# Optimization experiments

Hardware: AMD Instinct MI355X
Metric: run time of the kernel (lower is better)

## Reference

```python
import jax, jax.numpy as jnp
import numpy as np

# dims
T, B, N, H = 16, 8, 8, 128            # time, batch, num_schemas, schema_dim
C, IH, IW = 32, 16, 16                # conv_dims
TASK, ACT, REW = 128, 16, 1
HEADS = 7
TAR = TASK + ACT + REW                # 145
CTX = H + TAR                         # 273 context_dim
CONV_FLAT = C * IH * IW               # 8192
MEM_IN = CONV_FLAT + H + CTX          # 8593


def setup_inputs() -> dict:
    key = jax.random.key(0)
    ks = jax.random.split(key, 20)
    def n(k, shape, s=0.02):
        return jax.random.normal(k, shape, dtype=jnp.float32) * s
    D = HEADS * H
    return {
        "image": jax.random.normal(ks[0], (T, B, C, IH, IW), dtype=jnp.float32),
        "task_action_reward": jax.random.normal(ks[1], (T, B, TAR), dtype=jnp.float32),
        # MultiHeadedAttention params
        "Wq_w": n(ks[2], (D, CTX)), "Wq_b": jnp.zeros((D,), jnp.float32),
        "Wk_w": n(ks[3], (D, H)),   "Wk_b": jnp.zeros((D,), jnp.float32),
        "Wv_w": n(ks[4], (D, H)),   "Wv_b": jnp.zeros((D,), jnp.float32),
        "Wo_w": n(ks[5], (H, D)),   "Wo_b": jnp.zeros((H,), jnp.float32),
        # TopdownFeatureAttention: N per-query linears (stacked) + 1x1 conv
        "td_w": n(ks[6], (N, C, CTX)), "td_b": jnp.zeros((N, C), jnp.float32),
        "conv_w": n(ks[7], (C, C)), "conv_b": jnp.zeros((C,), jnp.float32),
        # ListStructuredRnn: N per-schema LSTM cells (PyTorch gate order i,f,g,o)
        "Wih": n(ks[8], (N, 4 * H, MEM_IN)), "Whh": n(ks[9], (N, 4 * H, H)),
        "bih": jnp.zeros((N, 4 * H), jnp.float32), "bhh": jnp.zeros((N, 4 * H), jnp.float32),
    }


def reference(image, task_action_reward, Wq_w, Wq_b, Wk_w, Wk_b, Wv_w, Wv_b,
              Wo_w, Wo_b, td_w, td_b, conv_w, conv_b, Wih, Whh, bih, bhh):
    f32 = image.dtype
    # prev_state=None path: prev_h is zeros for all timesteps
    prev_h = jnp.zeros((T, B, N, H), f32)
    # schema_context = duplicate task_action_reward over schemas, cat prev_h -> (T,B,N,CTX)
    ctx = jnp.concatenate(
        [jnp.broadcast_to(task_action_reward[:, :, None, :], (T, B, N, TAR)), prev_h], axis=-1)
    # keys = cat(prev_h, zeros) along schema axis -> (T,B,N+1,H)
    keys = jnp.concatenate([prev_h, jnp.zeros((T, B, 1, H), f32)], axis=2)

    # --- MultiHeadedAttention (no mask; dropout unused in forward) ---
    q = (ctx @ Wq_w.T + Wq_b).reshape(T, B, N, HEADS, H)
    k = (keys @ Wk_w.T + Wk_b).reshape(T, B, N + 1, HEADS, H)
    v = (keys @ Wv_w.T + Wv_b).reshape(T, B, N + 1, HEADS, H)
    scores = jnp.einsum('tbqhd,tbkhd->tbhqk', q, k) / jnp.sqrt(jnp.asarray(H, f32))
    attn = jax.nn.softmax(scores, axis=-1)
    xatt = jnp.einsum('tbhqk,tbkhd->tbqhd', attn, v).reshape(T, B, N, HEADS * H)
    shared = xatt @ Wo_w.T + Wo_b                      # (T,B,N,H)

    # --- TopdownFeatureAttention: per-query linear -> sigmoid channel gate -> 1x1 conv ---
    gate = jax.nn.sigmoid(jnp.einsum('tbnx,ncx->tbnc', ctx, td_w) + td_b)   # (T,B,N,C)
    modulated = image[:, :, None] * gate[..., None, None]                    # (T,B,N,C,IH,IW)
    conv = jnp.einsum('tbnchw,dc->tbndhw', modulated, conv_w) + conv_b[:, None, None]
    schema_updates = conv.reshape(T, B, N, CONV_FLAT)

    # --- per-schema LSTMs over time (zero initial state) ---
    mem = jnp.concatenate([schema_updates, shared, ctx], axis=-1)            # (T,B,N,MEM_IN)
    xg = jnp.einsum('tbni,ngi->tbng', mem, Wih) + bih + bhh                  # (T,B,N,4H)

    def step(carry, g_t):
        h, c = carry
        g = g_t + jnp.einsum('bnh,ngh->bng', h, Whh)
        i, f, gg, o = jnp.split(g, 4, axis=-1)
        c = jax.nn.sigmoid(f) * c + jax.nn.sigmoid(i) * jnp.tanh(gg)
        h = jax.nn.sigmoid(o) * jnp.tanh(c)
        return (h, c), h

    z = jnp.zeros((B, N, H), f32)
    (hT, cT), hs = jax.lax.scan(step, (z, z), xg)
    outs = hs.reshape(T, B, N * H)
    return outs, hT, cT
```

## Files before the change

kernel.cpp:

```cpp
#include <hip/hip_runtime.h>

#define T_   16
#define B_   8
#define N_   8
#define H_   128
#define C_   32
#define HW_  256
#define TAR_ 145
#define G4H  512
#define MEMIN 8593
#define AK   8512
#define XGN  524288
#define KSTEP 64

typedef __attribute__((ext_vector_type(8))) short short8v;
typedef __attribute__((ext_vector_type(4))) float f32x4;
typedef __attribute__((ext_vector_type(4), aligned(4))) float f32x4u;

__device__ __forceinline__ float bf2f(unsigned short u){
  return __uint_as_float(((unsigned int)u) << 16);
}
__device__ __forceinline__ unsigned short f2bf(float x){
  unsigned int b = __float_as_uint(x);
  return (unsigned short)((b + 0x7fffu + ((b >> 16) & 1u)) >> 16);
}
__device__ __forceinline__ unsigned pkbf(float lo, float hi){
  return __builtin_amdgcn_perm(__float_as_uint(hi) + 0x8000u,
                               __float_as_uint(lo) + 0x8000u, 0x07060302u);
}
__device__ __forceinline__ float bflo(unsigned w){ return __uint_as_float(w << 16); }
__device__ __forceinline__ float bfhi(unsigned w){ return __uint_as_float(w & 0xffff0000u); }
__device__ __forceinline__ float sigf(float x){ return 1.f/(1.f + expf(-x)); }

__device__ __forceinline__ void gl_lds16(const void* g, void* l){
  __builtin_amdgcn_global_load_lds(
      (const __attribute__((address_space(1))) unsigned int*)g,
      (__attribute__((address_space(3))) unsigned int*)l, 16, 0, 0);
}
__device__ __forceinline__ void gl_lds4(const void* g, void* l){
  __builtin_amdgcn_global_load_lds(
      (const __attribute__((address_space(1))) unsigned int*)g,
      (__attribute__((address_space(3))) unsigned int*)l, 4, 0, 0);
}

__global__ void k_shared(const float* __restrict__ WvB, const float* __restrict__ WoW,
                         const float* __restrict__ WoB, float* __restrict__ sh){
  const int h = blockIdx.x, lane = threadIdx.x;
  float acc = 0.f;
  for(int d = lane; d < 896; d += 64) acc += WvB[d] * WoW[h*896 + d];
  for(int s = 32; s; s >>= 1) acc += __shfl_down(acc, s);
  if(lane == 0) sh[h] = acc + WoB[h];
}

__global__ __launch_bounds__(256) void k_gate(const float* __restrict__ tar,
                                              const float* __restrict__ tdw,
                                              const float* __restrict__ tdb,
                                              float* __restrict__ gate){
  __shared__ float twS[32*145];
  __shared__ float taS[16*145];
  const int tb0 = blockIdx.x * 16, n = blockIdx.y, tid = threadIdx.x;
  for(int i = tid; i < 32*145; i += 256){
    int c = i / 145, x = i - c*145;
    twS[i] = tdw[(n*32 + c)*273 + x];
  }
  for(int i = tid; i < 16*145; i += 256)
    taS[i] = tar[tb0*145 + i];
  __syncthreads();
  for(int o = tid; o < 512; o += 256){
    int r = o >> 5, c = o & 31;
    float a = tdb[n*32 + c];
    const float* tr = &taS[r*145];
    const float* tw = &twS[c*145];
    for(int x = 0; x < 145; ++x) a += tr[x]*tw[x];
    gate[((tb0 + r)*N_ + n)*C_ + c] = 1.f/(1.f + expf(-a));
  }
}

__global__ __launch_bounds__(256) void k_conv2(
    const float* __restrict__ img, const float* __restrict__ gate,
    const float* __restrict__ cw, const float* __restrict__ cb,
    const float* __restrict__ sh, const float* __restrict__ tar,
    unsigned short* __restrict__ mem)
{
  __shared__ float imgS[8192];
  __shared__ float cwgT[1024];
  const int tb = blockIdx.x, n = blockIdx.y;
  const int hw = threadIdx.x;
  for(int i = hw; i < 8192; i += 256)
    imgS[i] = img[(size_t)tb*8192 + i];
  for(int i = hw; i < 1024; i += 256){
    const int c = i >> 5, d = i & 31;
    cwgT[i] = cw[d*32 + c] * gate[(tb*8 + n)*32 + c];
  }
  __syncthreads();
  f32x4 acc[8];
  #pragma unroll
  for(int dq = 0; dq < 8; ++dq){
    const f32x4u cv = *(const f32x4u*)&cb[dq*4];
    acc[dq].x = cv.x; acc[dq].y = cv.y; acc[dq].z = cv.z; acc[dq].w = cv.w;
  }
  #pragma unroll 4
  for(int c = 0; c < 32; ++c){
    const float iv = imgS[c*256 + hw];
    #pragma unroll
    for(int dq = 0; dq < 8; ++dq){
      const f32x4 w = *(const f32x4*)&cwgT[c*32 + dq*4];
      acc[dq].x += iv*w.x; acc[dq].y += iv*w.y;
      acc[dq].z += iv*w.z; acc[dq].w += iv*w.w;
    }
  }
  unsigned short* mrow = mem + (size_t)(n*128 + tb)*AK;
  #pragma unroll
  for(int dq = 0; dq < 8; ++dq){
    mrow[(dq*4 + 0)*256 + hw] = f2bf(acc[dq].x);
    mrow[(dq*4 + 1)*256 + hw] = f2bf(acc[dq].y);
    mrow[(dq*4 + 2)*256 + hw] = f2bf(acc[dq].z);
    mrow[(dq*4 + 3)*256 + hw] = f2bf(acc[dq].w);
  }
  for(int i = hw; i < 320; i += 256){
    if(i < 128)      mrow[8192 + i]       = f2bf(sh[i]);
    else if(i < 273) mrow[8320 + i - 128] = f2bf(tar[tb*TAR_ + i - 128]);
    else             mrow[8465 + i - 273] = 0;
  }
}

__global__ __launch_bounds__(256) void k_gemm7(
    const unsigned short* __restrict__ mem, const float* __restrict__ Wih,
    float* __restrict__ xg)
{
  extern __shared__ char smem7[];
  unsigned short (*Abuf)[128*64] = (unsigned short(*)[128*64])smem7;
  float (*Bbuf)[16*64] = (float(*)[16*64])(smem7 + 4*128*64*2);
  const int bid = blockIdx.x;
  const int n = bid & 7, gt = bid >> 3;
  const int tid = threadIdx.x;
  const int wv = tid >> 6, ln = tid & 63;
  const int lr = ln & 15, lg = ln >> 4;
  const int g0 = gt*16;
  const unsigned short* An = mem + (size_t)n*128*AK;
  const float* Bn = Wih + (size_t)(n*G4H + g0)*MEMIN;

#define STAGE7(sl, kk) do{                                                     \
    _Pragma("unroll")                                                          \
    for(int i_ = 0; i_ < 4; ++i_){                                             \
      const int ci_ = i_*256 + tid;                                            \
      const int row_ = ci_ >> 3;                                               \
      const unsigned short* src_ = An + (size_t)row_*AK + (kk)                 \
                                   + (((ci_ & 7) ^ (row_ & 7)) << 3);          \
      gl_lds16(src_, &Abuf[sl][(i_*256 + wv*64)*8]);                           \
    }                                                                          \
    _Pragma("unroll")                                                          \
    for(int q_ = 0; q_ < 4; ++q_){                                             \
      const int idx_ = q_*256 + tid;                                           \
      const int g_ = idx_ >> 6;                                                \
      const int kd_ = idx_ & 63;                                               \
      const float* srcB_ = Bn + (size_t)g_*MEMIN + (kk)                        \
                           + ((((kd_ >> 3) ^ (g_ & 7)) << 3) + (kd_ & 7));     \
      gl_lds4(srcB_, &Bbuf[sl][q_*256 + wv*64]);                               \
    }                                                                          \
  }while(0)

  f32x4 acc0 = {0.f,0.f,0.f,0.f};
  f32x4 acc1 = {0.f,0.f,0.f,0.f};

  STAGE7(0, 0);
  STAGE7(1, KSTEP);
  STAGE7(2, 2*KSTEP);

  for(int t = 0; t < 133; ++t){
    if(t < 131){
      asm volatile("s_waitcnt vmcnt(16)" ::: "memory");
    } else if(t == 131){
      asm volatile("s_waitcnt vmcnt(8)" ::: "memory");
    } else {
      asm volatile("s_waitcnt vmcnt(0)" ::: "memory");
    }
    __builtin_amdgcn_s_barrier();
    const int sl = t & 3;
    #pragma unroll
    for(int s = 0; s < 2; ++s){
      const int jb = (s*4 + lg) ^ (lr & 7);
      const float* bp = &Bbuf[sl][lr*64 + jb*8];
      const f32x4 blo = *(const f32x4*)bp;
      const f32x4 bhi = *(const f32x4*)(bp + 4);
      short8v bf;
      unsigned* u = (unsigned*)&bf;
      u[0] = pkbf(blo.x, blo.y); u[1] = pkbf(blo.z, blo.w);
      u[2] = pkbf(bhi.x, bhi.y); u[3] = pkbf(bhi.z, bhi.w);
      const short8v a0 = *(const short8v*)&Abuf[sl][(wv*32 + lr)*64 + jb*8];
      const short8v a1 = *(const short8v*)&Abuf[sl][(wv*32 + 16 + lr)*64 + jb*8];
      acc0 = __builtin_amdgcn_mfma_f32_16x16x32_bf16(a0, bf, acc0, 0, 0, 0);
      acc1 = __builtin_amdgcn_mfma_f32_16x16x32_bf16(a1, bf, acc1, 0, 0, 0);
    }
    if(t + 3 < 133) STAGE7((t + 3) & 3, (t + 3)*KSTEP);
  }
#undef STAGE7

  const int c0 = g0 + lr;
  const int r0 = wv*32 + lg*4, r1 = r0 + 16;
  #pragma unroll
  for(int j = 0; j < 4; ++j){
    xg[(size_t)((r0 + j)*8 + n)*G4H + c0] = acc0[j];
    xg[(size_t)((r1 + j)*8 + n)*G4H + c0] = acc1[j];
  }
}

__global__ __launch_bounds__(512) void k_lstm2(
    const float* __restrict__ xg4, int nsum, const float* __restrict__ Whh,
    const float* __restrict__ bih, const float* __restrict__ bhh,
    float* __restrict__ out)
{
  __shared__ float hS[128];
  __shared__ float preS[512];
  const int bn = blockIdx.x;
  const int n = bn & 7, b = bn >> 3;
  const int g = threadIdx.x;

  unsigned wr[64];
  const float* wrow = Whh + (size_t)(n*G4H + g)*H_;
  #pragma unroll
  for(int i = 0; i < 32; ++i){
    const f32x4 w = *(const f32x4*)(wrow + i*4);
    wr[2*i]   = pkbf(w.x, w.y);
    wr[2*i+1] = pkbf(w.z, w.w);
  }
  const float bias = bih[n*G4H + g] + bhh[n*G4H + g];
  if(g < 128) hS[g] = 0.f;
  float cc = 0.f;
  __syncthreads();

  for(int t = 0; t < 16; ++t){
    const size_t xb = (size_t)((t*8 + b)*8 + n)*G4H + g;
    float acc = bias;
    for(int u = 0; u < nsum; ++u) acc += xg4[xb + (size_t)u*XGN];
    #pragma unroll
    for(int q = 0; q < 32; ++q){
      const f32x4 hv = *(const f32x4*)&hS[q*4];
      const unsigned w0 = wr[2*q], w1 = wr[2*q+1];
      acc += hv.x*bflo(w0) + hv.y*bfhi(w0) + hv.z*bflo(w1) + hv.w*bfhi(w1);
    }
    preS[g] = acc;
    __syncthreads();
    if(g < 128){
      const float iv = sigf(preS[g]);
      const float fv = sigf(preS[128 + g]);
      const float gv = tanhf(preS[256 + g]);
      const float ov = sigf(preS[384 + g]);
      cc = fv*cc + iv*gv;
      const float hn = ov*tanhf(cc);
      hS[g] = hn;
      out[(t*8 + b)*1024 + n*128 + g] = hn;
      if(t == 15){
        out[131072 + (b*8 + n)*128 + g] = hn;
        out[139264 + (b*8 + n)*128 + g] = cc;
      }
    }
    __syncthreads();
  }
}

__global__ __launch_bounds__(256) void k_gemm5(
    const unsigned short* __restrict__ mem, const float* __restrict__ Wih,
    float* __restrict__ xg4)
{
  __shared__ unsigned short Abuf[2][128*64];
  __shared__ float          Bbuf[2][16*64];
  const int gt = blockIdx.x, n = blockIdx.y, ks = blockIdx.z;
  const int tid = threadIdx.x;
  const int wv = tid >> 6, ln = tid & 63;
  const int lr = ln & 15, lg = ln >> 4;
  const int g0 = gt*16;
  const int kbeg = (ks == 0) ? 0 : 2176 + (ks - 1)*2112;
  const int nsteps = (ks == 0) ? 34 : 33;
  const unsigned short* An = mem + (size_t)n*128*AK;
  const float* Bn = Wih + (size_t)(n*G4H + g0)*MEMIN;

#define STAGE5(bb, kk) do{                                                     \
    _Pragma("unroll")                                                          \
    for(int i_ = 0; i_ < 4; ++i_){                                             \
      const int ci_ = i_*256 + tid;                                            \
      const int row_ = ci_ >> 3;                                               \
      const unsigned short* src_ = An + (size_t)row_*AK + (kk)                 \
                                   + (((ci_ & 7) ^ (row_ & 7)) << 3);          \
      gl_lds16(src_, &Abuf[bb][(i_*256 + wv*64)*8]);                           \
    }                                                                          \
    _Pragma("unroll")                                                          \
    for(int q_ = 0; q_ < 4; ++q_){                                             \
      const int idx_ = q_*256 + tid;                                           \
      const int g_ = idx_ >> 6;                                                \
      const int kd_ = idx_ & 63;                                               \
      const float* srcB_ = Bn + (size_t)g_*MEMIN + (kk)                        \
                           + ((((kd_ >> 3) ^ (g_ & 7)) << 3) + (kd_ & 7));     \
      gl_lds4(srcB_, &Bbuf[bb][q_*256 + wv*64]);                               \
    }                                                                          \
  }while(0)

  f32x4 acc0 = {0.f,0.f,0.f,0.f};
  f32x4 acc1 = {0.f,0.f,0.f,0.f};

  STAGE5(0, kbeg);
  if(nsteps > 1) STAGE5(1, kbeg + KSTEP);

  int b = 0;
  for(int t = 0; t < nsteps; ++t){
    if(t < nsteps - 1){
      asm volatile("s_waitcnt vmcnt(8)" ::: "memory");
    } else {
      asm volatile("s_waitcnt vmcnt(0)" ::: "memory");
    }
    __builtin_amdgcn_s_barrier();
    #pragma unroll
    for(int s = 0; s < 2; ++s){
      const int jb = (s*4 + lg) ^ (lr & 7);
      const float* bp = &Bbuf[b][lr*64 + jb*8];
      const f32x4 blo = *(const f32x4*)bp;
      const f32x4 bhi = *(const f32x4*)(bp + 4);
      short8v bf;
      unsigned* u = (unsigned*)&bf;
      u[0] = pkbf(blo.x, blo.y); u[1] = pkbf(blo.z, blo.w);
      u[2] = pkbf(bhi.x, bhi.y); u[3] = pkbf(bhi.z, bhi.w);
      const short8v a0 = *(const short8v*)&Abuf[b][(wv*32 + lr)*64 + jb*8];
      const short8v a1 = *(const short8v*)&Abuf[b][(wv*32 + 16 + lr)*64 + jb*8];
      acc0 = __builtin_amdgcn_mfma_f32_16x16x32_bf16(a0, bf, acc0, 0, 0, 0);
      acc1 = __builtin_amdgcn_mfma_f32_16x16x32_bf16(a1, bf, acc1, 0, 0, 0);
    }
    __builtin_amdgcn_s_barrier();
    if(t + 2 < nsteps) STAGE5(b, kbeg + (t+2)*KSTEP);
    b ^= 1;
  }
#undef STAGE5

  float* dst = xg4 + (size_t)ks*XGN;
  const int c0 = g0 + lr;
  const int r0 = wv*32 + lg*4, r1 = r0 + 16;
  #pragma unroll
  for(int j = 0; j < 4; ++j){
    dst[(size_t)((r0 + j)*8 + n)*G4H + c0] = acc0[j];
    dst[(size_t)((r1 + j)*8 + n)*G4H + c0] = acc1[j];
  }
}

extern "C" void kernel_launch(void* const* d_in, const int* in_sizes, int n_in,
                              void* d_out, int out_size, void* d_ws, size_t ws_size,
                              hipStream_t stream)
{
  (void)in_sizes; (void)n_in; (void)out_size;
  const float* img  = (const float*)d_in[0];
  const float* tar  = (const float*)d_in[1];
  const float* WvB  = (const float*)d_in[7];
  const float* WoW  = (const float*)d_in[8];
  const float* WoB  = (const float*)d_in[9];
  const float* tdw  = (const float*)d_in[10];
  const float* tdb  = (const float*)d_in[11];
  const float* cw   = (const float*)d_in[12];
  const float* cb   = (const float*)d_in[13];
  const float* Wih  = (const float*)d_in[14];
  const float* Whh  = (const float*)d_in[15];
  const float* bih  = (const float*)d_in[16];
  const float* bhh  = (const float*)d_in[17];

  float* wsf   = (float*)d_ws;
  float* gatew = wsf;
  float* shw   = wsf + 32768;
  float* xgw   = wsf + 32896;
  unsigned short* memA = (unsigned short*)((char*)d_ws + 8520192);
  const size_t WS_7 = 8520192 + (size_t)8*128*AK*2;

  k_shared<<<128, 64, 0, stream>>>(WvB, WoW, WoB, shw);
  k_gate<<<dim3(8, 8), 256, 0, stream>>>(tar, tdw, tdb, gatew);
  k_conv2<<<dim3(128, 8), 256, 0, stream>>>(img, gatew, cw, cb, shw, tar, memA);

  if(ws_size >= WS_7){
    (void)hipFuncSetAttribute((const void*)k_gemm7,
                              hipFuncAttributeMaxDynamicSharedMemorySize, 81920);
    k_gemm7<<<256, 256, 81920, stream>>>(memA, Wih, xgw);
    k_lstm2<<<64, 512, 0, stream>>>(xgw, 1, Whh, bih, bhh, (float*)d_out);
  } else {
    k_gemm5<<<dim3(32, 8, 4), 256, 0, stream>>>(memA, Wih, xgw);
    k_lstm2<<<64, 512, 0, stream>>>(xgw, 4, Whh, bih, bhh, (float*)d_out);
  }
}
```

Measured before the change: 125.1 us.

## Widen GEMM tile to 64 gate columns with split-K over four partial outputs

Replaces the input-projection GEMM kernel with one in which each block computes 128 rows by 64 gate columns over a quarter of K, writing four partial sums that the LSTM kernel adds up (nsum=4). This lets each A tile in LDS feed eight MFMAs per wave instead of two, which cuts repeated A traffic, while split-K keeps the grid at 256 blocks. B rows are now loaded with 16-byte copies from unaligned row starts into a padded LDS layout. The cost is much more LDS per block (144KB), extra partial-sum memory traffic, and more reduction work in the LSTM kernel.

```diff
diff --git a/kernel.cpp b/kernel.cpp
--- a/kernel.cpp
+++ b/kernel.cpp
@@ -124,84 +124,94 @@
   }
 }
 
-__global__ __launch_bounds__(256) void k_gemm7(
+__global__ __launch_bounds__(256) void k_gemm8(
     const unsigned short* __restrict__ mem, const float* __restrict__ Wih,
-    float* __restrict__ xg)
-{
-  extern __shared__ char smem7[];
-  unsigned short (*Abuf)[128*64] = (unsigned short(*)[128*64])smem7;
-  float (*Bbuf)[16*64] = (float(*)[16*64])(smem7 + 4*128*64*2);
+    float* __restrict__ xg4)
+{
+  extern __shared__ char smem8[];
+  unsigned short (*Abuf)[8192] = (unsigned short(*)[8192])smem8;
+  float (*Bbuf)[5120] = (float(*)[5120])(smem8 + 4*16384);
   const int bid = blockIdx.x;
-  const int n = bid & 7, gt = bid >> 3;
+  const int n = bid & 7, r2 = bid >> 3;
+  const int gt = r2 & 7, ks = r2 >> 3;
   const int tid = threadIdx.x;
   const int wv = tid >> 6, ln = tid & 63;
   const int lr = ln & 15, lg = ln >> 4;
-  const int g0 = gt*16;
+  const int g0 = gt*64;
+  const int kbeg = (ks == 0) ? 0 : 2176 + (ks - 1)*2112;
+  const int nsteps = (ks == 0) ? 34 : 33;
   const unsigned short* An = mem + (size_t)n*128*AK;
-  const float* Bn = Wih + (size_t)(n*G4H + g0)*MEMIN;
-
-#define STAGE7(sl, kk) do{                                                     \
+  const int rbase = n*512 + g0 + wv*16;
+
+#define STAGE8(sl, kk) do{                                                     \
     _Pragma("unroll")                                                          \
     for(int i_ = 0; i_ < 4; ++i_){                                             \
       const int ci_ = i_*256 + tid;                                            \
       const int row_ = ci_ >> 3;                                               \
-      const unsigned short* src_ = An + (size_t)row_*AK + (kk)                 \
-                                   + (((ci_ & 7) ^ (row_ & 7)) << 3);          \
-      gl_lds16(src_, &Abuf[sl][(i_*256 + wv*64)*8]);                           \
+      gl_lds16(An + (size_t)row_*AK + (kk) + (((ci_ & 7) ^ (row_ & 7)) << 3),  \
+               (char*)&Abuf[sl][0] + (i_*256 + wv*64)*16);                     \
     }                                                                          \
     _Pragma("unroll")                                                          \
-    for(int q_ = 0; q_ < 4; ++q_){                                             \
-      const int idx_ = q_*256 + tid;                                           \
-      const int g_ = idx_ >> 6;                                                \
-      const int kd_ = idx_ & 63;                                               \
-      const float* srcB_ = Bn + (size_t)g_*MEMIN + (kk)                        \
-                           + ((((kd_ >> 3) ^ (g_ & 7)) << 3) + (kd_ & 7));     \
-      gl_lds4(srcB_, &Bbuf[sl][q_*256 + wv*64]);                               \
+    for(int o_ = 0; o_ < 5; ++o_){                                             \
+      const int p_ = o_*64 + ln;                                               \
+      int gl_ = p_ / 18;                                                       \
+      const int c_ = p_ - gl_*18;                                              \
+      if(gl_ > 15) gl_ = 15;                                                   \
+      const size_t ridx_ = (size_t)(rbase + gl_);                              \
+      const char* src_ = (const char*)Wih + ridx_*((size_t)MEMIN*4)            \
+                         + (size_t)(kk)*4 - ((ridx_ & 3)*4) + c_*16;           \
+      gl_lds16(src_, (char*)&Bbuf[sl][0] + wv*5120 + o_*1024);                 \
     }                                                                          \
   }while(0)
 
-  f32x4 acc0 = {0.f,0.f,0.f,0.f};
-  f32x4 acc1 = {0.f,0.f,0.f,0.f};
-
-  STAGE7(0, 0);
-  STAGE7(1, KSTEP);
-  STAGE7(2, 2*KSTEP);
-
-  for(int t = 0; t < 133; ++t){
-    if(t < 131){
-      asm volatile("s_waitcnt vmcnt(16)" ::: "memory");
-    } else if(t == 131){
-      asm volatile("s_waitcnt vmcnt(8)" ::: "memory");
+  f32x4 acc[8];
+  #pragma unroll
+  for(int rt = 0; rt < 8; ++rt){ acc[rt].x=0.f; acc[rt].y=0.f; acc[rt].z=0.f; acc[rt].w=0.f; }
+
+  STAGE8(0, kbeg);
+  STAGE8(1, kbeg + KSTEP);
+  STAGE8(2, kbeg + 2*KSTEP);
+
+  for(int t = 0; t < nsteps; ++t){
+    if(t < nsteps - 2){
+      asm volatile("s_waitcnt vmcnt(18)" ::: "memory");
+    } else if(t == nsteps - 2){
+      asm volatile("s_waitcnt vmcnt(9)" ::: "memory");
     } else {
       asm volatile("s_waitcnt vmcnt(0)" ::: "memory");
     }
     __builtin_amdgcn_s_barrier();
     const int sl = t & 3;
+    const char* Ab = (const char*)&Abuf[sl][0];
     #pragma unroll
     for(int s = 0; s < 2; ++s){
-      const int jb = (s*4 + lg) ^ (lr & 7);
-      const float* bp = &Bbuf[sl][lr*64 + jb*8];
-      const f32x4 blo = *(const f32x4*)bp;
-      const f32x4 bhi = *(const f32x4*)(bp + 4);
+      const int u = s*4 + lg;
+      const int fb = wv*1280 + lr*72 + (lr & 3) + u*8;
+      const f32x4u blo = *(const f32x4u*)&Bbuf[sl][fb];
+      const f32x4u bhi = *(const f32x4u*)&Bbuf[sl][fb + 4];
       short8v bf;
-      unsigned* u = (unsigned*)&bf;
-      u[0] = pkbf(blo.x, blo.y); u[1] = pkbf(blo.z, blo.w);
-      u[2] = pkbf(bhi.x, bhi.y); u[3] = pkbf(bhi.z, bhi.w);
-      const short8v a0 = *(const short8v*)&Abuf[sl][(wv*32 + lr)*64 + jb*8];
-      const short8v a1 = *(const short8v*)&Abuf[sl][(wv*32 + 16 + lr)*64 + jb*8];
-      acc0 = __builtin_amdgcn_mfma_f32_16x16x32_bf16(a0, bf, acc0, 0, 0, 0);
-      acc1 = __builtin_amdgcn_mfma_f32_16x16x32_bf16(a1, bf, acc1, 0, 0, 0);
-    }
-    if(t + 3 < 133) STAGE7((t + 3) & 3, (t + 3)*KSTEP);
-  }
-#undef STAGE7
-
-  const int c0 = g0 + lr;
-  const int r0 = wv*32 + lg*4, r1 = r0 + 16;
-  #pragma unroll
-  for(int j = 0; j < 4; ++j){
-    xg[(size_t)((r0 + j)*8 + n)*G4H + c0] = acc0[j];
-    xg[(size_t)((r1 + j)*8 + n)*G4H + c0] = acc1[j];
+      unsigned* up = (unsigned*)&bf;
+      up[0] = pkbf(blo.x, blo.y); up[1] = pkbf(blo.z, blo.w);
+      up[2] = pkbf(bhi.x, bhi.y); up[3] = pkbf(bhi.z, bhi.w);
+      const int jbx = u ^ (lr & 7);
+      #pragma unroll
+      for(int rt = 0; rt < 8; ++rt){
+        const short8v a = *(const short8v*)(Ab + (((rt*16 + lr)*8 + jbx) << 4));
+        acc[rt] = __builtin_amdgcn_mfma_f32_16x16x32_bf16(a, bf, acc[rt], 0, 0, 0);
+      }
+    }
+    if(t + 3 < nsteps) STAGE8((t + 3) & 3, kbeg + (t + 3)*KSTEP);
+  }
+#undef STAGE8
+
+  float* dst = xg4 + (size_t)ks*XGN;
+  const int col = g0 + wv*16 + lr;
+  #pragma unroll
+  for(int rt = 0; rt < 8; ++rt){
+    #pragma unroll
+    for(int j = 0; j < 4; ++j){
+      dst[(size_t)((rt*16 + lg*4 + j)*8 + n)*G4H + col] = acc[rt][j];
+    }
   }
 }
 
@@ -371,10 +381,10 @@
   k_conv2<<<dim3(128, 8), 256, 0, stream>>>(img, gatew, cw, cb, shw, tar, memA);
 
   if(ws_size >= WS_7){
-    (void)hipFuncSetAttribute((const void*)k_gemm7,
-                              hipFuncAttributeMaxDynamicSharedMemorySize, 81920);
-    k_gemm7<<<256, 256, 81920, stream>>>(memA, Wih, xgw);
-    k_lstm2<<<64, 512, 0, stream>>>(xgw, 1, Whh, bih, bhh, (float*)d_out);
+    (void)hipFuncSetAttribute((const void*)k_gemm8,
+                              hipFuncAttributeMaxDynamicSharedMemorySize, 147456);
+    k_gemm8<<<256, 256, 147456, stream>>>(memA, Wih, xgw);
+    k_lstm2<<<64, 512, 0, stream>>>(xgw, 4, Whh, bih, bhh, (float*)d_out);
   } else {
     k_gemm5<<<dim3(32, 8, 4), 256, 0, stream>>>(memA, Wih, xgw);
     k_lstm2<<<64, 512, 0, stream>>>(xgw, 4, Whh, bih, bhh, (float*)d_out);
```

Result: faster. 122.5 us (-2.0%).

## Fuse gate into conv kernel and always use split-K GEMM with flattened grid

Applied to the files above, without the earlier changes.

The channel-gate computation is folded into the conv kernel: each block computes its 32 sigmoid gates from the task/action/reward row staged in LDS, which removes the separate k_gate launch and its global round trip. The 4-stage single-pass k_gemm7 path is dropped. The 4-way split-K GEMM now always runs, on a flattened 1024-block grid with the schema index varying fastest, and the LSTM sums the four partial gate tensors. This trades a deeper per-block pipeline for more blocks in flight, at the cost of extra partial-sum traffic and redundant gate dot products per block.

```diff
diff --git a/kernel.cpp b/kernel.cpp
--- a/kernel.cpp
+++ b/kernel.cpp
@@ -52,47 +52,38 @@
   if(lane == 0) sh[h] = acc + WoB[h];
 }
 
-__global__ __launch_bounds__(256) void k_gate(const float* __restrict__ tar,
-                                              const float* __restrict__ tdw,
-                                              const float* __restrict__ tdb,
-                                              float* __restrict__ gate){
-  __shared__ float twS[32*145];
-  __shared__ float taS[16*145];
-  const int tb0 = blockIdx.x * 16, n = blockIdx.y, tid = threadIdx.x;
-  for(int i = tid; i < 32*145; i += 256){
-    int c = i / 145, x = i - c*145;
-    twS[i] = tdw[(n*32 + c)*273 + x];
-  }
-  for(int i = tid; i < 16*145; i += 256)
-    taS[i] = tar[tb0*145 + i];
-  __syncthreads();
-  for(int o = tid; o < 512; o += 256){
-    int r = o >> 5, c = o & 31;
-    float a = tdb[n*32 + c];
-    const float* tr = &taS[r*145];
-    const float* tw = &twS[c*145];
-    for(int x = 0; x < 145; ++x) a += tr[x]*tw[x];
-    gate[((tb0 + r)*N_ + n)*C_ + c] = 1.f/(1.f + expf(-a));
-  }
-}
-
-__global__ __launch_bounds__(256) void k_conv2(
-    const float* __restrict__ img, const float* __restrict__ gate,
+__global__ __launch_bounds__(256) void k_conv3(
+    const float* __restrict__ img, const float* __restrict__ tar,
+    const float* __restrict__ tdw, const float* __restrict__ tdb,
     const float* __restrict__ cw, const float* __restrict__ cb,
-    const float* __restrict__ sh, const float* __restrict__ tar,
-    unsigned short* __restrict__ mem)
+    const float* __restrict__ sh, unsigned short* __restrict__ mem)
 {
   __shared__ float imgS[8192];
   __shared__ float cwgT[1024];
-  const int tb = blockIdx.x, n = blockIdx.y;
+  __shared__ float tarS[160];
+  __shared__ float gateS[32];
+  const int bid = blockIdx.x;
+  const int n = bid & 7, tb = bid >> 3;
   const int hw = threadIdx.x;
+
+  if(hw < 145) tarS[hw] = tar[tb*TAR_ + hw];
   for(int i = hw; i < 8192; i += 256)
     imgS[i] = img[(size_t)tb*8192 + i];
+  __syncthreads();
+  if(hw < 32){
+    float a = tdb[n*32 + hw];
+    const float* tw = tdw + (size_t)(n*32 + hw)*273;
+    #pragma unroll 5
+    for(int x = 0; x < 145; ++x) a += tarS[x]*tw[x];
+    gateS[hw] = sigf(a);
+  }
+  __syncthreads();
   for(int i = hw; i < 1024; i += 256){
     const int c = i >> 5, d = i & 31;
-    cwgT[i] = cw[d*32 + c] * gate[(tb*8 + n)*32 + c];
-  }
-  __syncthreads();
+    cwgT[i] = cw[d*32 + c] * gateS[c];
+  }
+  __syncthreads();
+
   f32x4 acc[8];
   #pragma unroll
   for(int dq = 0; dq < 8; ++dq){
@@ -119,153 +110,21 @@
   }
   for(int i = hw; i < 320; i += 256){
     if(i < 128)      mrow[8192 + i]       = f2bf(sh[i]);
-    else if(i < 273) mrow[8320 + i - 128] = f2bf(tar[tb*TAR_ + i - 128]);
+    else if(i < 273) mrow[8320 + i - 128] = f2bf(tarS[i - 128]);
     else             mrow[8465 + i - 273] = 0;
   }
 }
 
-__global__ __launch_bounds__(256) void k_gemm7(
-    const unsigned short* __restrict__ mem, const float* __restrict__ Wih,
-    float* __restrict__ xg)
-{
-  extern __shared__ char smem7[];
-  unsigned short (*Abuf)[128*64] = (unsigned short(*)[128*64])smem7;
-  float (*Bbuf)[16*64] = (float(*)[16*64])(smem7 + 4*128*64*2);
-  const int bid = blockIdx.x;
-  const int n = bid & 7, gt = bid >> 3;
-  const int tid = threadIdx.x;
-  const int wv = tid >> 6, ln = tid & 63;
-  const int lr = ln & 15, lg = ln >> 4;
-  const int g0 = gt*16;
-  const unsigned short* An = mem + (size_t)n*128*AK;
-  const float* Bn = Wih + (size_t)(n*G4H + g0)*MEMIN;
-
-#define STAGE7(sl, kk) do{                                                     \
-    _Pragma("unroll")                                                          \
-    for(int i_ = 0; i_ < 4; ++i_){                                             \
-      const int ci_ = i_*256 + tid;                                            \
-      const int row_ = ci_ >> 3;                                               \
-      const unsigned short* src_ = An + (size_t)row_*AK + (kk)                 \
-                                   + (((ci_ & 7) ^ (row_ & 7)) << 3);          \
-      gl_lds16(src_, &Abuf[sl][(i_*256 + wv*64)*8]);                           \
-    }                                                                          \
-    _Pragma("unroll")                                                          \
-    for(int q_ = 0; q_ < 4; ++q_){                                             \
-      const int idx_ = q_*256 + tid;                                           \
-      const int g_ = idx_ >> 6;                                                \
-      const int kd_ = idx_ & 63;                                               \
-      const float* srcB_ = Bn + (size_t)g_*MEMIN + (kk)                        \
-                           + ((((kd_ >> 3) ^ (g_ & 7)) << 3) + (kd_ & 7));     \
-      gl_lds4(srcB_, &Bbuf[sl][q_*256 + wv*64]);                               \
-    }                                                                          \
-  }while(0)
-
-  f32x4 acc0 = {0.f,0.f,0.f,0.f};
-  f32x4 acc1 = {0.f,0.f,0.f,0.f};
-
-  STAGE7(0, 0);
-  STAGE7(1, KSTEP);
-  STAGE7(2, 2*KSTEP);
-
-  for(int t = 0; t < 133; ++t){
-    if(t < 131){
-      asm volatile("s_waitcnt vmcnt(16)" ::: "memory");
-    } else if(t == 131){
-      asm volatile("s_waitcnt vmcnt(8)" ::: "memory");
-    } else {
-      asm volatile("s_waitcnt vmcnt(0)" ::: "memory");
-    }
-    __builtin_amdgcn_s_barrier();
-    const int sl = t & 3;
-    #pragma unroll
-    for(int s = 0; s < 2; ++s){
-      const int jb = (s*4 + lg) ^ (lr & 7);
-      const float* bp = &Bbuf[sl][lr*64 + jb*8];
-      const f32x4 blo = *(const f32x4*)bp;
-      const f32x4 bhi = *(const f32x4*)(bp + 4);
-      short8v bf;
-      unsigned* u = (unsigned*)&bf;
-      u[0] = pkbf(blo.x, blo.y); u[1] = pkbf(blo.z, blo.w);
-      u[2] = pkbf(bhi.x, bhi.y); u[3] = pkbf(bhi.z, bhi.w);
-      const short8v a0 = *(const short8v*)&Abuf[sl][(wv*32 + lr)*64 + jb*8];
-      const short8v a1 = *(const short8v*)&Abuf[sl][(wv*32 + 16 + lr)*64 + jb*8];
-      acc0 = __builtin_amdgcn_mfma_f32_16x16x32_bf16(a0, bf, acc0, 0, 0, 0);
-      acc1 = __builtin_amdgcn_mfma_f32_16x16x32_bf16(a1, bf, acc1, 0, 0, 0);
-    }
-    if(t + 3 < 133) STAGE7((t + 3) & 3, (t + 3)*KSTEP);
-  }
-#undef STAGE7
-
-  const int c0 = g0 + lr;
-  const int r0 = wv*32 + lg*4, r1 = r0 + 16;
-  #pragma unroll
-  for(int j = 0; j < 4; ++j){
-    xg[(size_t)((r0 + j)*8 + n)*G4H + c0] = acc0[j];
-    xg[(size_t)((r1 + j)*8 + n)*G4H + c0] = acc1[j];
-  }
-}
-
-__global__ __launch_bounds__(512) void k_lstm2(
-    const float* __restrict__ xg4, int nsum, const float* __restrict__ Whh,
-    const float* __restrict__ bih, const float* __restrict__ bhh,
-    float* __restrict__ out)
-{
-  __shared__ float hS[128];
-  __shared__ float preS[512];
-  const int bn = blockIdx.x;
-  const int n = bn & 7, b = bn >> 3;
-  const int g = threadIdx.x;
-
-  unsigned wr[64];
-  const float* wrow = Whh + (size_t)(n*G4H + g)*H_;
-  #pragma unroll
-  for(int i = 0; i < 32; ++i){
-    const f32x4 w = *(const f32x4*)(wrow + i*4);
-    wr[2*i]   = pkbf(w.x, w.y);
-    wr[2*i+1] = pkbf(w.z, w.w);
-  }
-  const float bias = bih[n*G4H + g] + bhh[n*G4H + g];
-  if(g < 128) hS[g] = 0.f;
-  float cc = 0.f;
-  __syncthreads();
-
-  for(int t = 0; t < 16; ++t){
-    const size_t xb = (size_t)((t*8 + b)*8 + n)*G4H + g;
-    float acc = bias;
-    for(int u = 0; u < nsum; ++u) acc += xg4[xb + (size_t)u*XGN];
-    #pragma unroll
-    for(int q = 0; q < 32; ++q){
-      const f32x4 hv = *(const f32x4*)&hS[q*4];
-      const unsigned w0 = wr[2*q], w1 = wr[2*q+1];
-      acc += hv.x*bflo(w0) + hv.y*bfhi(w0) + hv.z*bflo(w1) + hv.w*bfhi(w1);
-    }
-    preS[g] = acc;
-    __syncthreads();
-    if(g < 128){
-      const float iv = sigf(preS[g]);
-      const float fv = sigf(preS[128 + g]);
-      const float gv = tanhf(preS[256 + g]);
-      const float ov = sigf(preS[384 + g]);
-      cc = fv*cc + iv*gv;
-      const float hn = ov*tanhf(cc);
-      hS[g] = hn;
-      out[(t*8 + b)*1024 + n*128 + g] = hn;
-      if(t == 15){
-        out[131072 + (b*8 + n)*128 + g] = hn;
-        out[139264 + (b*8 + n)*128 + g] = cc;
-      }
-    }
-    __syncthreads();
-  }
-}
-
-__global__ __launch_bounds__(256) void k_gemm5(
+__global__ __launch_bounds__(256) void k_gemm5x(
     const unsigned short* __restrict__ mem, const float* __restrict__ Wih,
     float* __restrict__ xg4)
 {
   __shared__ unsigned short Abuf[2][128*64];
   __shared__ float          Bbuf[2][16*64];
-  const int gt = blockIdx.x, n = blockIdx.y, ks = blockIdx.z;
+  const int bid = blockIdx.x;
+  const int n = bid & 7;
+  const int r2 = bid >> 3;
+  const int gt = r2 & 31, ks = r2 >> 5;
   const int tid = threadIdx.x;
   const int wv = tid >> 6, ln = tid & 63;
   const int lr = ln & 15, lg = ln >> 4;
@@ -340,11 +199,65 @@
   }
 }
 
+__global__ __launch_bounds__(512) void k_lstm2(
+    const float* __restrict__ xg4, int nsum, const float* __restrict__ Whh,
+    const float* __restrict__ bih, const float* __restrict__ bhh,
+    float* __restrict__ out)
+{
+  __shared__ float hS[128];
+  __shared__ float preS[512];
+  const int bn = blockIdx.x;
+  const int n = bn & 7, b = bn >> 3;
+  const int g = threadIdx.x;
+
+  unsigned wr[64];
+  const float* wrow = Whh + (size_t)(n*G4H + g)*H_;
+  #pragma unroll
+  for(int i = 0; i < 32; ++i){
+    const f32x4 w = *(const f32x4*)(wrow + i*4);
+    wr[2*i]   = pkbf(w.x, w.y);
+    wr[2*i+1] = pkbf(w.z, w.w);
+  }
+  const float bias = bih[n*G4H + g] + bhh[n*G4H + g];
+  if(g < 128) hS[g] = 0.f;
+  float cc = 0.f;
+  __syncthreads();
+
+  for(int t = 0; t < 16; ++t){
+    const size_t xb = (size_t)((t*8 + b)*8 + n)*G4H + g;
+    float acc = bias;
+    for(int u = 0; u < nsum; ++u) acc += xg4[xb + (size_t)u*XGN];
+    #pragma unroll
+    for(int q = 0; q < 32; ++q){
+      const f32x4 hv = *(const f32x4*)&hS[q*4];
+      const unsigned w0 = wr[2*q], w1 = wr[2*q+1];
+      acc += hv.x*bflo(w0) + hv.y*bfhi(w0) + hv.z*bflo(w1) + hv.w*bfhi(w1);
+    }
+    preS[g] = acc;
+    __syncthreads();
+    if(g < 128){
+      const float iv = sigf(preS[g]);
+      const float fv = sigf(preS[128 + g]);
+      const float gv = tanhf(preS[256 + g]);
+      const float ov = sigf(preS[384 + g]);
+      cc = fv*cc + iv*gv;
+      const float hn = ov*tanhf(cc);
+      hS[g] = hn;
+      out[(t*8 + b)*1024 + n*128 + g] = hn;
+      if(t == 15){
+        out[131072 + (b*8 + n)*128 + g] = hn;
+        out[139264 + (b*8 + n)*128 + g] = cc;
+      }
+    }
+    __syncthreads();
+  }
+}
+
 extern "C" void kernel_launch(void* const* d_in, const int* in_sizes, int n_in,
                               void* d_out, int out_size, void* d_ws, size_t ws_size,
                               hipStream_t stream)
 {
-  (void)in_sizes; (void)n_in; (void)out_size;
+  (void)in_sizes; (void)n_in; (void)out_size; (void)ws_size;
   const float* img  = (const float*)d_in[0];
   const float* tar  = (const float*)d_in[1];
   const float* WvB  = (const float*)d_in[7];
@@ -359,24 +272,13 @@
   const float* bih  = (const float*)d_in[16];
   const float* bhh  = (const float*)d_in[17];
 
-  float* wsf   = (float*)d_ws;
-  float* gatew = wsf;
-  float* shw   = wsf + 32768;
-  float* xgw   = wsf + 32896;
+  float* wsf = (float*)d_ws;
+  float* shw = wsf + 32768;
+  float* xgw = wsf + 32896;
   unsigned short* memA = (unsigned short*)((char*)d_ws + 8520192);
-  const size_t WS_7 = 8520192 + (size_t)8*128*AK*2;
 
   k_shared<<<128, 64, 0, stream>>>(WvB, WoW, WoB, shw);
-  k_gate<<<dim3(8, 8), 256, 0, stream>>>(tar, tdw, tdb, gatew);
-  k_conv2<<<dim3(128, 8), 256, 0, stream>>>(img, gatew, cw, cb, shw, tar, memA);
-
-  if(ws_size >= WS_7){
-    (void)hipFuncSetAttribute((const void*)k_gemm7,
-                              hipFuncAttributeMaxDynamicSharedMemorySize, 81920);
-    k_gemm7<<<256, 256, 81920, stream>>>(memA, Wih, xgw);
-    k_lstm2<<<64, 512, 0, stream>>>(xgw, 1, Whh, bih, bhh, (float*)d_out);
-  } else {
-    k_gemm5<<<dim3(32, 8, 4), 256, 0, stream>>>(memA, Wih, xgw);
-    k_lstm2<<<64, 512, 0, stream>>>(xgw, 4, Whh, bih, bhh, (float*)d_out);
-  }
-}
+  k_conv3<<<1024, 256, 0, stream>>>(img, tar, tdw, tdb, cw, cb, shw, memA);
+  k_gemm5x<<<1024, 256, 0, stream>>>(memA, Wih, xgw);
+  k_lstm2<<<64, 512, 0, stream>>>(xgw, 4, Whh, bih, bhh, (float*)d_out);
+}
```

Measured after the change: 117.8 us, median of 2. -5.8%, faster.
